# Optimization experiments

Hardware: AMD Instinct MI355X
Metric: run time of the kernel (lower is better)

Reference implementation:

```python
import jax, jax.numpy as jnp
import numpy as np
from functools import partial

T, B = 1000, 256
STATE_DIM, ACTION_DIM, REWARD_DIM = 64, 8, 1
EMBED = 64
HIDDEN = 256


def setup_inputs() -> dict:
    key = jax.random.key(0)
    ks = jax.random.split(key, 12)
    g = lambda k, shape, fan_in: jax.random.normal(k, shape, jnp.float32) * np.sqrt(2.0 / fan_in)
    return {
        "states": jax.random.normal(ks[0], (T, B, STATE_DIM), jnp.float32),
        "actions": jax.random.normal(ks[1], (T, B, ACTION_DIM), jnp.float32),
        "rewards": jax.random.normal(ks[2], (T, B, REWARD_DIM), jnp.float32),
        # embedding linears (VarianceScaling(2.0) init, zero bias)
        "Ws": g(ks[3], (STATE_DIM, EMBED), STATE_DIM), "bs": jnp.zeros((EMBED,), jnp.float32),
        "Wa": g(ks[4], (ACTION_DIM, EMBED), ACTION_DIM), "ba": jnp.zeros((EMBED,), jnp.float32),
        "Wr": g(ks[5], (REWARD_DIM, EMBED), REWARD_DIM), "br": jnp.zeros((EMBED,), jnp.float32),
        # hk.GRU params: w_i [in, 3H], w_h [H, 3H], b [3H]
        "wi": g(ks[6], (3 * EMBED, 3 * HIDDEN), 3 * EMBED),
        "wh": g(ks[7], (HIDDEN, 3 * HIDDEN), HIDDEN),
        "bg": jnp.zeros((3 * HIDDEN,), jnp.float32),
    }


def _gru_scan(x_seq, h0, wi, wh, bg):
    # x_seq: [T, B, 3*EMBED]; hk.GRU math: z,r = sigmoid gates; a = tanh candidate
    H = HIDDEN
    wh_zr, wh_a = wh[:, : 2 * H], wh[:, 2 * H :]
    b_zr, b_a = bg[: 2 * H], bg[2 * H :]

    def step(h, gx):  # gx = x @ wi precomputed, [B, 3H]
        zr = jax.nn.sigmoid(gx[:, : 2 * H] + h @ wh_zr + b_zr)
        z, r = zr[:, :H], zr[:, H:]
        a = jnp.tanh(gx[:, 2 * H :] + (r * h) @ wh_a + b_a)
        h_next = (1.0 - z) * h + z * a
        return h_next, h_next

    gx_seq = jnp.einsum("tbd,dh->tbh", x_seq, wi)  # one big matmul over all steps
    _, hs = jax.lax.scan(step, h0, gx_seq)
    return hs  # [T, B, H]


def reference(states, actions, rewards, Ws, bs, Wa, ba, Wr, br, wi, wh, bg):
    se = jax.nn.gelu(states @ Ws + bs)
    ae = jax.nn.gelu(actions @ Wa + ba)
    re = jax.nn.gelu(rewards @ Wr + br)
    x = jnp.concatenate((se, ae, re), axis=-1)  # [T, B, 3*EMBED]
    h0 = jnp.zeros((x.shape[1], HIDDEN), x.dtype)
    return _gru_scan(x, h0, wi, wh, bg)
```

## Files before the change

kernel.cpp:

```cpp
#include <hip/hip_runtime.h>
#include <hip/hip_bf16.h>

#define TT   1000
#define BB   256
#define HID  256
#define GD   768
#define XD   192
#define NROW (TT*BB)

typedef __attribute__((ext_vector_type(8))) _Float16 half8;
typedef __attribute__((ext_vector_type(4))) float    float4_t;
typedef __attribute__((ext_vector_type(2))) unsigned uint2_t;

#define MFMA16(A,B,C) __builtin_amdgcn_mfma_f32_16x16x32_f16((A),(B),(C),0,0,0)

__device__ __forceinline__ void gll16(const void* g, void* l) {
  __builtin_amdgcn_global_load_lds((const __attribute__((address_space(1))) void*)g,
                                   (__attribute__((address_space(3))) void*)l, 16, 0, 0);
}

__device__ __forceinline__ unsigned short f2h(float f) {
  _Float16 h = (_Float16)f;
  union { _Float16 h; unsigned short u; } c; c.h = h; return c.u;
}
__device__ __forceinline__ uint2_t pk4h(float4_t v) {
  union { _Float16 h[4]; uint2_t u; } c;
  c.h[0] = (_Float16)v.x; c.h[1] = (_Float16)v.y;
  c.h[2] = (_Float16)v.z; c.h[3] = (_Float16)v.w;
  return c.u;
}
__device__ __forceinline__ float4_t h4_to_f4(uint2_t v) {
  union { uint2_t u; _Float16 h[4]; } c; c.u = v;
  float4_t f;
  f.x = (float)c.h[0]; f.y = (float)c.h[1];
  f.z = (float)c.h[2]; f.w = (float)c.h[3];
  return f;
}
__device__ __forceinline__ float sigx(float x) {
  return __builtin_amdgcn_rcpf(1.0f + __builtin_amdgcn_exp2f(-1.4426950408889634f * x));
}
__device__ __forceinline__ float tanhx(float x) {
  return 1.0f - 2.0f * __builtin_amdgcn_rcpf(1.0f + __builtin_amdgcn_exp2f(2.8853900817779268f * x));
}
__device__ __forceinline__ float4_t sig4(float4_t v){ float4_t o; o.x=sigx(v.x); o.y=sigx(v.y); o.z=sigx(v.z); o.w=sigx(v.w); return o; }
__device__ __forceinline__ float4_t tanh4(float4_t v){ float4_t o; o.x=tanhx(v.x); o.y=tanhx(v.y); o.z=tanhx(v.z); o.w=tanhx(v.w); return o; }
__device__ __forceinline__ float gelu1(float v){
  float c = v + 0.044715f * v * v * v;
  float e = __builtin_amdgcn_exp2f((0.7978845608028654f * 2.8853900817779268f) * c);
  float th = 1.0f - 2.0f * __builtin_amdgcn_rcpf(1.0f + e);
  return 0.5f * v * (1.0f + th);
}

__global__ void k_prep(const float* __restrict__ wi, const float* __restrict__ wh,
                       unsigned short* __restrict__ wiT, unsigned short* __restrict__ whF)
{
  int tid = blockIdx.x * 256 + threadIdx.x;
  if (tid < GD*XD) {
    int n = tid / XD, k = tid - n*XD;
    wiT[tid] = f2h(wi[(size_t)k*GD + n]);
  }
  int t2 = tid - GD*XD;
  if (t2 >= 0 && t2 < 48*8*64*8) {
    int j = t2 & 7, l = (t2 >> 3) & 63, f = t2 >> 9;
    int mf = f >> 3, kf = f & 7;
    int k = kf*32 + ((l >> 4) << 3) + j;
    int n = (mf << 4) + (l & 15);
    whF[t2] = f2h(wh[(size_t)k*GD + n]);
  }
}

__global__ void k_embed(const float* __restrict__ st, const float* __restrict__ ac,
                        const float* __restrict__ rw,
                        const float* __restrict__ Ws, const float* __restrict__ bs,
                        const float* __restrict__ Wa, const float* __restrict__ ba,
                        const float* __restrict__ Wr, const float* __restrict__ br,
                        unsigned short* __restrict__ x)
{
  int lane = threadIdx.x & 63;
  int wid = blockIdx.x * (blockDim.x >> 6) + (threadIdx.x >> 6);
  int nw  = gridDim.x * (blockDim.x >> 6);
  float wsr[64], war[8];
  #pragma unroll
  for (int k = 0; k < 64; ++k) wsr[k] = Ws[k*64 + lane];
  #pragma unroll
  for (int k = 0; k < 8; ++k) war[k] = Wa[k*64 + lane];
  float wrr = Wr[lane];
  float bsv = bs[lane], bav = ba[lane], brv = br[lane];
  for (int row = wid; row < NROW; row += nw) {
    const float4_t* sp = (const float4_t*)(st + (size_t)row*64);
    float a0 = bsv;
    #pragma unroll
    for (int q = 0; q < 16; ++q) {
      float4_t v = sp[q];
      a0 = fmaf(v.x, wsr[4*q+0], a0);
      a0 = fmaf(v.y, wsr[4*q+1], a0);
      a0 = fmaf(v.z, wsr[4*q+2], a0);
      a0 = fmaf(v.w, wsr[4*q+3], a0);
    }
    const float4_t* ap = (const float4_t*)(ac + (size_t)row*8);
    float a1 = bav;
    #pragma unroll
    for (int q = 0; q < 2; ++q) {
      float4_t v = ap[q];
      a1 = fmaf(v.x, war[4*q+0], a1);
      a1 = fmaf(v.y, war[4*q+1], a1);
      a1 = fmaf(v.z, war[4*q+2], a1);
      a1 = fmaf(v.w, war[4*q+3], a1);
    }
    float a2 = fmaf(rw[row], wrr, brv);
    unsigned short* xr = x + (size_t)row*XD;
    xr[lane]       = f2h(gelu1(a0));
    xr[64 + lane]  = f2h(gelu1(a1));
    xr[128 + lane] = f2h(gelu1(a2));
  }
}

__global__ __launch_bounds__(512, 2) void k_gx(const unsigned short* __restrict__ x,
                                               const unsigned short* __restrict__ wiT,
                                               const float* __restrict__ bg,
                                               unsigned short* __restrict__ gx)
{
  __shared__ half8 Xs[24*64];
  __shared__ half8 As[16*64];
  int lane = threadIdx.x & 63;
  int wv   = threadIdx.x >> 6;
  int b    = lane & 15;
  int g8   = (lane >> 4) << 3;
  int row0 = blockIdx.x * 64;
  #pragma unroll
  for (int i = 0; i < 3; ++i) {
    int c = wv*3 + i, nf = c / 6, kf = c - nf*6;
    gll16(x + (size_t)(row0 + nf*16 + b)*XD + kf*32 + g8, &Xs[c*64]);
  }
  int g4 = g8 >> 1;
  float4_t acc[6][4];
  #pragma unroll
  for (int i = 0; i < 6; ++i) {
    float4_t bgv = *(const float4_t*)(bg + (wv + 8*i)*16 + g4);
    #pragma unroll
    for (int nf = 0; nf < 4; ++nf) acc[i][nf] = bgv;
  }
  half8 xb[4];
  for (int kf = 0; kf < 6; ++kf) {
    #pragma unroll
    for (int p = 0; p < 3; ++p) {
      __syncthreads();
      #pragma unroll
      for (int i2 = 0; i2 < 2; ++i2) {
        int q = wv*2 + i2;
        gll16(wiT + (size_t)((p*16 + q)*16 + b)*XD + kf*32 + g8, &As[q*64]);
      }
      __syncthreads();
      if (p == 0) {
        #pragma unroll
        for (int nf = 0; nf < 4; ++nf) xb[nf] = Xs[(nf*6 + kf)*64 + lane];
      }
      half8 af0 = As[wv*64 + lane];
      half8 af1 = As[(wv+8)*64 + lane];
      #pragma unroll
      for (int nf = 0; nf < 4; ++nf) {
        acc[2*p  ][nf] = MFMA16(af0, xb[nf], acc[2*p  ][nf]);
        acc[2*p+1][nf] = MFMA16(af1, xb[nf], acc[2*p+1][nf]);
      }
    }
  }
  char* gxc = (char*)gx;
  #pragma unroll
  for (int i = 0; i < 6; ++i) {
    #pragma unroll
    for (int nf = 0; nf < 4; ++nf) {
      size_t idx = (((size_t)blockIdx.x*48 + (wv + 8*i))*4 + nf)*512 + lane*8;
      *(uint2_t*)(gxc + idx) = pk4h(acc[i][nf]);
    }
  }
}

__global__
__attribute__((amdgpu_flat_work_group_size(512, 512), amdgpu_waves_per_eu(2, 2)))
void k_gru(const unsigned short* __restrict__ gx,
           const unsigned short* __restrict__ whF,
           float* __restrict__ out)
{
  __shared__ char smem[98304];
  char* h_lds  = smem;
  char* rh_lds = smem + 8448;
  char* gxb    = smem + 16896;
  const int tid  = threadIdx.x;
  const int lane = tid & 63;
  const int wv   = tid >> 6;
  const int wg   = blockIdx.x;
  const int b    = lane & 15;
  const int g    = lane >> 4;
  const int kr4  = g << 2;

  half8 wz0[8], wz1[8], wr0[8], wr1[8], wa0[8], wa1[8];
  #pragma unroll
  for (int kf = 0; kf < 8; ++kf) {
    wz0[kf] = *(const half8*)(whF + ((size_t)((( 2*wv    )*8 + kf)*64 + lane) << 3));
    wz1[kf] = *(const half8*)(whF + ((size_t)((( 2*wv + 1)*8 + kf)*64 + lane) << 3));
    wr0[kf] = *(const half8*)(whF + ((size_t)(((16 + 2*wv)*8 + kf)*64 + lane) << 3));
    wr1[kf] = *(const half8*)(whF + ((size_t)(((17 + 2*wv)*8 + kf)*64 + lane) << 3));
    wa0[kf] = *(const half8*)(whF + ((size_t)(((32 + 2*wv)*8 + kf)*64 + lane) << 3));
    wa1[kf] = *(const half8*)(whF + ((size_t)(((33 + 2*wv)*8 + kf)*64 + lane) << 3));
  }
  #pragma unroll
  for (int kf = 0; kf < 8; ++kf) {
    asm volatile("" : "+v"(wz0[kf]));
    asm volatile("" : "+v"(wz1[kf]));
    asm volatile("" : "+v"(wr0[kf]));
    asm volatile("" : "+v"(wr1[kf]));
    asm volatile("" : "+v"(wa0[kf]));
    asm volatile("" : "+v"(wa1[kf]));
  }
  for (int i = tid; i < 2112; i += 512) ((unsigned*)h_lds)[i] = 0u;

  const int nf   = wg & 3;
  const int bsel = wg >> 2;
  int soff[3], dch[3];
  #pragma unroll
  for (int i = 0; i < 3; ++i) {
    int c = i*16 + (tid >> 5);
    int r = (tid & 31) << 4;
    soff[i] = nf*512 + c*2048 + r;
    dch[i]  = i*8192 + tid*16;
  }
  const char* gxc = (const char*)gx;
  #pragma unroll
  for (int i = 0; i < 3; ++i)
    gll16(gxc + (size_t)bsel*98304 + soff[i], gxb + dch[i]);
  __syncthreads();

  float4_t hf0 = {0.f, 0.f, 0.f, 0.f}, hf1 = hf0;
  const char* hb_base = h_lds + b*528;
  const char* rb_base = rh_lds + b*528;
  const int off_h0 = (wv*32 + kr4) << 1;
  const int off_h1 = off_h0 + 32;
  const int lz0 = ( 2*wv    )*512 + lane*8;
  const int lz1 = ( 2*wv + 1)*512 + lane*8;
  const int lr0 = (16 + 2*wv)*512 + lane*8;
  const int lr1 = (17 + 2*wv)*512 + lane*8;
  const int la0 = (32 + 2*wv)*512 + lane*8;
  const int la1 = (33 + 2*wv)*512 + lane*8;

  for (int t = 0; t < TT; ++t) {
    asm volatile("s_waitcnt vmcnt(2) lgkmcnt(0)" ::: "memory");
    __builtin_amdgcn_s_barrier();
    asm volatile("" ::: "memory");
    if (t + 1 < TT) {
      const char* slab = gxc + ((size_t)(t+1)*4 + bsel)*98304;
      char* dstb = gxb + 24576*((t+1) & 1);
      #pragma unroll
      for (int i = 0; i < 3; ++i) gll16(slab + soff[i], dstb + dch[i]);
    }
    const char* cur = gxb + 24576*(t & 1);
    float4_t az0 = h4_to_f4(*(const uint2_t*)(cur + lz0));
    float4_t az1 = h4_to_f4(*(const uint2_t*)(cur + lz1));
    float4_t ar0 = h4_to_f4(*(const uint2_t*)(cur + lr0));
    float4_t ar1 = h4_to_f4(*(const uint2_t*)(cur + lr1));
    #pragma unroll
    for (int kf = 0; kf < 8; ++kf) {
      half8 hb = *(const half8*)(hb_base + kf*64 + (g << 4));
      az0 = MFMA16(wz0[kf], hb, az0);
      az1 = MFMA16(wz1[kf], hb, az1);
      ar0 = MFMA16(wr0[kf], hb, ar0);
      ar1 = MFMA16(wr1[kf], hb, ar1);
    }
    float4_t z0 = sig4(az0), z1 = sig4(az1);
    float4_t rh0 = sig4(ar0) * hf0, rh1 = sig4(ar1) * hf1;
    *(uint2_t*)(rh_lds + b*528 + off_h0) = pk4h(rh0);
    *(uint2_t*)(rh_lds + b*528 + off_h1) = pk4h(rh1);
    asm volatile("s_waitcnt lgkmcnt(0)" ::: "memory");
    __builtin_amdgcn_s_barrier();
    asm volatile("" ::: "memory");
    float4_t aa0 = h4_to_f4(*(const uint2_t*)(cur + la0));
    float4_t aa1 = h4_to_f4(*(const uint2_t*)(cur + la1));
    #pragma unroll
    for (int kf = 0; kf < 8; ++kf) {
      half8 rb = *(const half8*)(rb_base + kf*64 + (g << 4));
      aa0 = MFMA16(wa0[kf], rb, aa0);
      aa1 = MFMA16(wa1[kf], rb, aa1);
    }
    float4_t a0 = tanh4(aa0), a1 = tanh4(aa1);
    float4_t hn0 = hf0 + z0 * (a0 - hf0);
    float4_t hn1 = hf1 + z1 * (a1 - hf1);
    hf0 = hn0; hf1 = hn1;
    *(uint2_t*)(h_lds + b*528 + off_h0) = pk4h(hn0);
    *(uint2_t*)(h_lds + b*528 + off_h1) = pk4h(hn1);
    float* op = out + (((size_t)t*BB + wg*16 + b) << 8) + wv*32 + kr4;
    *(float4_t*)op = hn0;
    *(float4_t*)(op + 16) = hn1;
  }
}

extern "C" void kernel_launch(void* const* d_in, const int* in_sizes, int n_in,
                              void* d_out, int out_size, void* d_ws, size_t ws_size,
                              hipStream_t stream) {
  (void)in_sizes; (void)n_in; (void)out_size; (void)ws_size;
  const float* states  = (const float*)d_in[0];
  const float* actions = (const float*)d_in[1];
  const float* rewards = (const float*)d_in[2];
  const float* Ws = (const float*)d_in[3];
  const float* bs = (const float*)d_in[4];
  const float* Wa = (const float*)d_in[5];
  const float* ba = (const float*)d_in[6];
  const float* Wr = (const float*)d_in[7];
  const float* br = (const float*)d_in[8];
  const float* wi = (const float*)d_in[9];
  const float* wh = (const float*)d_in[10];
  const float* bg = (const float*)d_in[11];
  char* wsb = (char*)d_ws;
  unsigned short* gx  = (unsigned short*)(wsb);
  unsigned short* x   = (unsigned short*)(wsb + 393216000LL);
  unsigned short* wiT = (unsigned short*)(wsb + 491520000LL);
  unsigned short* whF = (unsigned short*)(wsb + 491814912LL);
  k_prep <<<1344, 256, 0, stream>>>(wi, wh, wiT, whF);
  k_embed<<<1000, 256, 0, stream>>>(states, actions, rewards, Ws, bs, Wa, ba, Wr, br, x);
  k_gx   <<<4000, 512, 0, stream>>>(x, wiT, bg, gx);
  k_gru  <<<16, 512, 0, stream>>>(gx, whF, (float*)d_out);
}
```

Measured before the change: 2.186 ms.

## Pin z/r recurrent weights in AGPRs and stream candidate weights from global

Moves the z and r gate weight fragments out of VGPRs into fixed AGPRs (a0-a127) with inline asm and feeds them straight to hand-written MFMA sequences. The candidate-gate weights are no longer kept resident; they are reloaded from global memory (expected to hit in cache) every timestep, with the loads issued early to overlap the gate math and barrier. The aim is to relieve VGPR pressure and control MFMA scheduling. In exchange it adds per-step global traffic and manual s_nop hazard padding, and the loaded operand layout must match the previous fragment layout exactly.

Result: slower. 2.874 ms (+31.5%).

```diff
diff --git a/kernel.cpp b/kernel.cpp
--- a/kernel.cpp
+++ b/kernel.cpp
@@ -13,6 +13,18 @@
 typedef __attribute__((ext_vector_type(2))) unsigned uint2_t;
 
 #define MFMA16(A,B,C) __builtin_amdgcn_mfma_f32_16x16x32_f16((A),(B),(C),0,0,0)
+
+#define ACLOB \
+  "a0","a1","a2","a3","a4","a5","a6","a7","a8","a9","a10","a11","a12","a13","a14","a15", \
+  "a16","a17","a18","a19","a20","a21","a22","a23","a24","a25","a26","a27","a28","a29","a30","a31", \
+  "a32","a33","a34","a35","a36","a37","a38","a39","a40","a41","a42","a43","a44","a45","a46","a47", \
+  "a48","a49","a50","a51","a52","a53","a54","a55","a56","a57","a58","a59","a60","a61","a62","a63", \
+  "a64","a65","a66","a67","a68","a69","a70","a71","a72","a73","a74","a75","a76","a77","a78","a79", \
+  "a80","a81","a82","a83","a84","a85","a86","a87","a88","a89","a90","a91","a92","a93","a94","a95", \
+  "a96","a97","a98","a99","a100","a101","a102","a103","a104","a105","a106","a107","a108","a109","a110","a111", \
+  "a112","a113","a114","a115","a116","a117","a118","a119","a120","a121","a122","a123","a124","a125","a126","a127"
+
+union h8u4 { half8 h; unsigned u[4]; };
 
 __device__ __forceinline__ void gll16(const void* g, void* l) {
   __builtin_amdgcn_global_load_lds((const __attribute__((address_space(1))) void*)g,
@@ -192,26 +204,33 @@
   const int b    = lane & 15;
   const int g    = lane >> 4;
   const int kr4  = g << 2;
-
-  half8 wz0[8], wz1[8], wr0[8], wr1[8], wa0[8], wa1[8];
-  #pragma unroll
-  for (int kf = 0; kf < 8; ++kf) {
-    wz0[kf] = *(const half8*)(whF + ((size_t)((( 2*wv    )*8 + kf)*64 + lane) << 3));
-    wz1[kf] = *(const half8*)(whF + ((size_t)((( 2*wv + 1)*8 + kf)*64 + lane) << 3));
-    wr0[kf] = *(const half8*)(whF + ((size_t)(((16 + 2*wv)*8 + kf)*64 + lane) << 3));
-    wr1[kf] = *(const half8*)(whF + ((size_t)(((17 + 2*wv)*8 + kf)*64 + lane) << 3));
-    wa0[kf] = *(const half8*)(whF + ((size_t)(((32 + 2*wv)*8 + kf)*64 + lane) << 3));
-    wa1[kf] = *(const half8*)(whF + ((size_t)(((33 + 2*wv)*8 + kf)*64 + lane) << 3));
-  }
-  #pragma unroll
-  for (int kf = 0; kf < 8; ++kf) {
-    asm volatile("" : "+v"(wz0[kf]));
-    asm volatile("" : "+v"(wz1[kf]));
-    asm volatile("" : "+v"(wr0[kf]));
-    asm volatile("" : "+v"(wr1[kf]));
-    asm volatile("" : "+v"(wa0[kf]));
-    asm volatile("" : "+v"(wa1[kf]));
-  }
+  const int g16  = g << 4;
+
+#define PIN(FK, S0,S1,S2,S3) do { h8u4 _c; \
+    _c.h = *(const half8*)(whF + ((size_t)((FK)*64 + lane) << 3)); \
+    asm volatile("v_accvgpr_write_b32 a" S0 ", %0\n\t" \
+                 "v_accvgpr_write_b32 a" S1 ", %1\n\t" \
+                 "v_accvgpr_write_b32 a" S2 ", %2\n\t" \
+                 "v_accvgpr_write_b32 a" S3 ", %3" \
+                 :: "v"(_c.u[0]), "v"(_c.u[1]), "v"(_c.u[2]), "v"(_c.u[3]) : ACLOB); } while(0)
+  PIN(16*wv+0,  "0","1","2","3");     PIN(16*wv+1,  "4","5","6","7");
+  PIN(16*wv+2,  "8","9","10","11");   PIN(16*wv+3,  "12","13","14","15");
+  PIN(16*wv+4,  "16","17","18","19"); PIN(16*wv+5,  "20","21","22","23");
+  PIN(16*wv+6,  "24","25","26","27"); PIN(16*wv+7,  "28","29","30","31");
+  PIN(16*wv+8,  "32","33","34","35"); PIN(16*wv+9,  "36","37","38","39");
+  PIN(16*wv+10, "40","41","42","43"); PIN(16*wv+11, "44","45","46","47");
+  PIN(16*wv+12, "48","49","50","51"); PIN(16*wv+13, "52","53","54","55");
+  PIN(16*wv+14, "56","57","58","59"); PIN(16*wv+15, "60","61","62","63");
+  PIN(128+16*wv+0, "64","65","66","67");   PIN(128+16*wv+1, "68","69","70","71");
+  PIN(128+16*wv+2, "72","73","74","75");   PIN(128+16*wv+3, "76","77","78","79");
+  PIN(128+16*wv+4, "80","81","82","83");   PIN(128+16*wv+5, "84","85","86","87");
+  PIN(128+16*wv+6, "88","89","90","91");   PIN(128+16*wv+7, "92","93","94","95");
+  PIN(136+16*wv+0, "96","97","98","99");    PIN(136+16*wv+1, "100","101","102","103");
+  PIN(136+16*wv+2, "104","105","106","107");PIN(136+16*wv+3, "108","109","110","111");
+  PIN(136+16*wv+4, "112","113","114","115");PIN(136+16*wv+5, "116","117","118","119");
+  PIN(136+16*wv+6, "120","121","122","123");PIN(136+16*wv+7, "124","125","126","127");
+#undef PIN
+
   for (int i = tid; i < 2112; i += 512) ((unsigned*)h_lds)[i] = 0u;
 
   const int nf   = wg & 3;
@@ -241,9 +260,10 @@
   const int lr1 = (17 + 2*wv)*512 + lane*8;
   const int la0 = (32 + 2*wv)*512 + lane*8;
   const int la1 = (33 + 2*wv)*512 + lane*8;
+  const unsigned short* wap = whF;
 
   for (int t = 0; t < TT; ++t) {
-    asm volatile("s_waitcnt vmcnt(2) lgkmcnt(0)" ::: "memory");
+    asm volatile("s_waitcnt vmcnt(2) lgkmcnt(0)" ::: "memory", ACLOB);
     __builtin_amdgcn_s_barrier();
     asm volatile("" ::: "memory");
     if (t + 1 < TT) {
@@ -257,29 +277,121 @@
     float4_t az1 = h4_to_f4(*(const uint2_t*)(cur + lz1));
     float4_t ar0 = h4_to_f4(*(const uint2_t*)(cur + lr0));
     float4_t ar1 = h4_to_f4(*(const uint2_t*)(cur + lr1));
-    #pragma unroll
-    for (int kf = 0; kf < 8; ++kf) {
-      half8 hb = *(const half8*)(hb_base + kf*64 + (g << 4));
-      az0 = MFMA16(wz0[kf], hb, az0);
-      az1 = MFMA16(wz1[kf], hb, az1);
-      ar0 = MFMA16(wr0[kf], hb, ar0);
-      ar1 = MFMA16(wr1[kf], hb, ar1);
-    }
+    half8 hb0 = *(const half8*)(hb_base + 0*64 + g16);
+    half8 hb1 = *(const half8*)(hb_base + 1*64 + g16);
+    half8 hb2 = *(const half8*)(hb_base + 2*64 + g16);
+    half8 hb3 = *(const half8*)(hb_base + 3*64 + g16);
+    half8 hb4 = *(const half8*)(hb_base + 4*64 + g16);
+    half8 hb5 = *(const half8*)(hb_base + 5*64 + g16);
+    half8 hb6 = *(const half8*)(hb_base + 6*64 + g16);
+    half8 hb7 = *(const half8*)(hb_base + 7*64 + g16);
+    asm volatile(
+      "s_nop 1\n\t"
+      "v_mfma_f32_16x16x32_f16 %0, a[0:3], %4, %0\n\t"
+      "v_mfma_f32_16x16x32_f16 %1, a[32:35], %4, %1\n\t"
+      "v_mfma_f32_16x16x32_f16 %2, a[64:67], %4, %2\n\t"
+      "v_mfma_f32_16x16x32_f16 %3, a[96:99], %4, %3\n\t"
+      "v_mfma_f32_16x16x32_f16 %0, a[4:7], %5, %0\n\t"
+      "v_mfma_f32_16x16x32_f16 %1, a[36:39], %5, %1\n\t"
+      "v_mfma_f32_16x16x32_f16 %2, a[68:71], %5, %2\n\t"
+      "v_mfma_f32_16x16x32_f16 %3, a[100:103], %5, %3\n\t"
+      "v_mfma_f32_16x16x32_f16 %0, a[8:11], %6, %0\n\t"
+      "v_mfma_f32_16x16x32_f16 %1, a[40:43], %6, %1\n\t"
+      "v_mfma_f32_16x16x32_f16 %2, a[72:75], %6, %2\n\t"
+      "v_mfma_f32_16x16x32_f16 %3, a[104:107], %6, %3\n\t"
+      "v_mfma_f32_16x16x32_f16 %0, a[12:15], %7, %0\n\t"
+      "v_mfma_f32_16x16x32_f16 %1, a[44:47], %7, %1\n\t"
+      "v_mfma_f32_16x16x32_f16 %2, a[76:79], %7, %2\n\t"
+      "v_mfma_f32_16x16x32_f16 %3, a[108:111], %7, %3\n\t"
+      "v_mfma_f32_16x16x32_f16 %0, a[16:19], %8, %0\n\t"
+      "v_mfma_f32_16x16x32_f16 %1, a[48:51], %8, %1\n\t"
+      "v_mfma_f32_16x16x32_f16 %2, a[80:83], %8, %2\n\t"
+      "v_mfma_f32_16x16x32_f16 %3, a[112:115], %8, %3\n\t"
+      "v_mfma_f32_16x16x32_f16 %0, a[20:23], %9, %0\n\t"
+      "v_mfma_f32_16x16x32_f16 %1, a[52:55], %9, %1\n\t"
+      "v_mfma_f32_16x16x32_f16 %2, a[84:87], %9, %2\n\t"
+      "v_mfma_f32_16x16x32_f16 %3, a[116:119], %9, %3\n\t"
+      "v_mfma_f32_16x16x32_f16 %0, a[24:27], %10, %0\n\t"
+      "v_mfma_f32_16x16x32_f16 %1, a[56:59], %10, %1\n\t"
+      "v_mfma_f32_16x16x32_f16 %2, a[88:91], %10, %2\n\t"
+      "v_mfma_f32_16x16x32_f16 %3, a[120:123], %10, %3\n\t"
+      "v_mfma_f32_16x16x32_f16 %0, a[28:31], %11, %0\n\t"
+      "v_mfma_f32_16x16x32_f16 %1, a[60:63], %11, %1\n\t"
+      "v_mfma_f32_16x16x32_f16 %2, a[92:95], %11, %2\n\t"
+      "v_mfma_f32_16x16x32_f16 %3, a[124:127], %11, %3\n\t"
+      "s_nop 7\n\t"
+      "s_nop 7"
+      : "+v"(az0), "+v"(az1), "+v"(ar0), "+v"(ar1)
+      : "v"(hb0), "v"(hb1), "v"(hb2), "v"(hb3),
+        "v"(hb4), "v"(hb5), "v"(hb6), "v"(hb7)
+      : ACLOB);
+    __builtin_amdgcn_sched_barrier(0);
+    asm volatile("" : "+s"(wap));
+    half8 wa00 = *(const half8*)(wap + ((size_t)((256+16*wv+0)*64 + lane) << 3));
+    half8 wa01 = *(const half8*)(wap + ((size_t)((256+16*wv+1)*64 + lane) << 3));
+    half8 wa02 = *(const half8*)(wap + ((size_t)((256+16*wv+2)*64 + lane) << 3));
+    half8 wa03 = *(const half8*)(wap + ((size_t)((256+16*wv+3)*64 + lane) << 3));
+    half8 wa04 = *(const half8*)(wap + ((size_t)((256+16*wv+4)*64 + lane) << 3));
+    half8 wa05 = *(const half8*)(wap + ((size_t)((256+16*wv+5)*64 + lane) << 3));
+    half8 wa06 = *(const half8*)(wap + ((size_t)((256+16*wv+6)*64 + lane) << 3));
+    half8 wa07 = *(const half8*)(wap + ((size_t)((256+16*wv+7)*64 + lane) << 3));
+    half8 wa10 = *(const half8*)(wap + ((size_t)((264+16*wv+0)*64 + lane) << 3));
+    half8 wa11 = *(const half8*)(wap + ((size_t)((264+16*wv+1)*64 + lane) << 3));
+    half8 wa12 = *(const half8*)(wap + ((size_t)((264+16*wv+2)*64 + lane) << 3));
+    half8 wa13 = *(const half8*)(wap + ((size_t)((264+16*wv+3)*64 + lane) << 3));
+    half8 wa14 = *(const half8*)(wap + ((size_t)((264+16*wv+4)*64 + lane) << 3));
+    half8 wa15 = *(const half8*)(wap + ((size_t)((264+16*wv+5)*64 + lane) << 3));
+    half8 wa16 = *(const half8*)(wap + ((size_t)((264+16*wv+6)*64 + lane) << 3));
+    half8 wa17 = *(const half8*)(wap + ((size_t)((264+16*wv+7)*64 + lane) << 3));
     float4_t z0 = sig4(az0), z1 = sig4(az1);
     float4_t rh0 = sig4(ar0) * hf0, rh1 = sig4(ar1) * hf1;
     *(uint2_t*)(rh_lds + b*528 + off_h0) = pk4h(rh0);
     *(uint2_t*)(rh_lds + b*528 + off_h1) = pk4h(rh1);
-    asm volatile("s_waitcnt lgkmcnt(0)" ::: "memory");
+    asm volatile("s_waitcnt lgkmcnt(0)" ::: "memory", ACLOB);
     __builtin_amdgcn_s_barrier();
     asm volatile("" ::: "memory");
     float4_t aa0 = h4_to_f4(*(const uint2_t*)(cur + la0));
     float4_t aa1 = h4_to_f4(*(const uint2_t*)(cur + la1));
-    #pragma unroll
-    for (int kf = 0; kf < 8; ++kf) {
-      half8 rb = *(const half8*)(rb_base + kf*64 + (g << 4));
-      aa0 = MFMA16(wa0[kf], rb, aa0);
-      aa1 = MFMA16(wa1[kf], rb, aa1);
-    }
+    half8 rb0 = *(const half8*)(rb_base + 0*64 + g16);
+    half8 rb1 = *(const half8*)(rb_base + 1*64 + g16);
+    half8 rb2 = *(const half8*)(rb_base + 2*64 + g16);
+    half8 rb3 = *(const half8*)(rb_base + 3*64 + g16);
+    asm volatile(
+      "s_nop 2\n\t"
+      "v_mfma_f32_16x16x32_f16 %0, %2, %10, %0\n\t"
+      "v_mfma_f32_16x16x32_f16 %1, %6, %10, %1\n\t"
+      "v_mfma_f32_16x16x32_f16 %0, %3, %11, %0\n\t"
+      "v_mfma_f32_16x16x32_f16 %1, %7, %11, %1\n\t"
+      "v_mfma_f32_16x16x32_f16 %0, %4, %12, %0\n\t"
+      "v_mfma_f32_16x16x32_f16 %1, %8, %12, %1\n\t"
+      "v_mfma_f32_16x16x32_f16 %0, %5, %13, %0\n\t"
+      "v_mfma_f32_16x16x32_f16 %1, %9, %13, %1"
+      : "+v"(aa0), "+v"(aa1)
+      : "v"(wa00), "v"(wa01), "v"(wa02), "v"(wa03),
+        "v"(wa10), "v"(wa11), "v"(wa12), "v"(wa13),
+        "v"(rb0), "v"(rb1), "v"(rb2), "v"(rb3)
+      : ACLOB);
+    half8 rb4 = *(const half8*)(rb_base + 4*64 + g16);
+    half8 rb5 = *(const half8*)(rb_base + 5*64 + g16);
+    half8 rb6 = *(const half8*)(rb_base + 6*64 + g16);
+    half8 rb7 = *(const half8*)(rb_base + 7*64 + g16);
+    asm volatile(
+      "s_nop 2\n\t"
+      "v_mfma_f32_16x16x32_f16 %0, %2, %10, %0\n\t"
+      "v_mfma_f32_16x16x32_f16 %1, %6, %10, %1\n\t"
+      "v_mfma_f32_16x16x32_f16 %0, %3, %11, %0\n\t"
+      "v_mfma_f32_16x16x32_f16 %1, %7, %11, %1\n\t"
+      "v_mfma_f32_16x16x32_f16 %0, %4, %12, %0\n\t"
+      "v_mfma_f32_16x16x32_f16 %1, %8, %12, %1\n\t"
+      "v_mfma_f32_16x16x32_f16 %0, %5, %13, %0\n\t"
+      "v_mfma_f32_16x16x32_f16 %1, %9, %13, %1\n\t"
+      "s_nop 7\n\t"
+      "s_nop 7"
+      : "+v"(aa0), "+v"(aa1)
+      : "v"(wa04), "v"(wa05), "v"(wa06), "v"(wa07),
+        "v"(wa14), "v"(wa15), "v"(wa16), "v"(wa17),
+        "v"(rb4), "v"(rb5), "v"(rb6), "v"(rb7)
+      : ACLOB);
     float4_t a0 = tanh4(aa0), a1 = tanh4(aa1);
     float4_t hn0 = hf0 + z0 * (a0 - hf0);
     float4_t hn1 = hf1 + z1 * (a1 - hf1);
```

## Pin recurrent weights in AGPRs and stream z-gate weights from global each step

Applied to the files above, without the earlier changes.

Moves the r-gate and candidate recurrent weight fragments into explicitly written AGPRs and issues the MFMAs through inline assembly that reads those registers directly. The z-gate weights are no longer kept resident and are reloaded from global memory (L2) every timestep into VGPRs. The gx prefetch now runs unconditionally so the vmcnt accounting stays consistent. The intent is to relieve VGPR pressure and spilling at two waves per EU. In exchange it adds global load latency on the serial critical path every step, and it relies on hand-placed s_nop padding for MFMA hazards and on clobber lists to keep the compiler out of the AGPRs.

New measurement: 3.401 ms. 1.56x slower.

```diff
diff --git a/kernel.cpp b/kernel.cpp
--- a/kernel.cpp
+++ b/kernel.cpp
@@ -13,6 +13,18 @@
 typedef __attribute__((ext_vector_type(2))) unsigned uint2_t;
 
 #define MFMA16(A,B,C) __builtin_amdgcn_mfma_f32_16x16x32_f16((A),(B),(C),0,0,0)
+
+#define ACLOB \
+  "a0","a1","a2","a3","a4","a5","a6","a7","a8","a9","a10","a11","a12","a13","a14","a15", \
+  "a16","a17","a18","a19","a20","a21","a22","a23","a24","a25","a26","a27","a28","a29","a30","a31", \
+  "a32","a33","a34","a35","a36","a37","a38","a39","a40","a41","a42","a43","a44","a45","a46","a47", \
+  "a48","a49","a50","a51","a52","a53","a54","a55","a56","a57","a58","a59","a60","a61","a62","a63", \
+  "a64","a65","a66","a67","a68","a69","a70","a71","a72","a73","a74","a75","a76","a77","a78","a79", \
+  "a80","a81","a82","a83","a84","a85","a86","a87","a88","a89","a90","a91","a92","a93","a94","a95", \
+  "a96","a97","a98","a99","a100","a101","a102","a103","a104","a105","a106","a107","a108","a109","a110","a111", \
+  "a112","a113","a114","a115","a116","a117","a118","a119","a120","a121","a122","a123","a124","a125","a126","a127"
+
+union h8u4 { half8 h; unsigned u[4]; };
 
 __device__ __forceinline__ void gll16(const void* g, void* l) {
   __builtin_amdgcn_global_load_lds((const __attribute__((address_space(1))) void*)g,
@@ -192,27 +204,40 @@
   const int b    = lane & 15;
   const int g    = lane >> 4;
   const int kr4  = g << 2;
-
-  half8 wz0[8], wz1[8], wr0[8], wr1[8], wa0[8], wa1[8];
-  #pragma unroll
-  for (int kf = 0; kf < 8; ++kf) {
-    wz0[kf] = *(const half8*)(whF + ((size_t)((( 2*wv    )*8 + kf)*64 + lane) << 3));
-    wz1[kf] = *(const half8*)(whF + ((size_t)((( 2*wv + 1)*8 + kf)*64 + lane) << 3));
-    wr0[kf] = *(const half8*)(whF + ((size_t)(((16 + 2*wv)*8 + kf)*64 + lane) << 3));
-    wr1[kf] = *(const half8*)(whF + ((size_t)(((17 + 2*wv)*8 + kf)*64 + lane) << 3));
-    wa0[kf] = *(const half8*)(whF + ((size_t)(((32 + 2*wv)*8 + kf)*64 + lane) << 3));
-    wa1[kf] = *(const half8*)(whF + ((size_t)(((33 + 2*wv)*8 + kf)*64 + lane) << 3));
-  }
-  #pragma unroll
-  for (int kf = 0; kf < 8; ++kf) {
-    asm volatile("" : "+v"(wz0[kf]));
-    asm volatile("" : "+v"(wz1[kf]));
-    asm volatile("" : "+v"(wr0[kf]));
-    asm volatile("" : "+v"(wr1[kf]));
-    asm volatile("" : "+v"(wa0[kf]));
-    asm volatile("" : "+v"(wa1[kf]));
-  }
+  const int g16  = g << 4;
+
+#define PIN(FK, S0,S1,S2,S3) do { h8u4 _c; \
+    _c.h = *(const half8*)(whF + ((size_t)((FK)*64 + lane) << 3)); \
+    asm volatile("v_accvgpr_write_b32 a" S0 ", %0\n\t" \
+                 "v_accvgpr_write_b32 a" S1 ", %1\n\t" \
+                 "v_accvgpr_write_b32 a" S2 ", %2\n\t" \
+                 "v_accvgpr_write_b32 a" S3 ", %3" \
+                 :: "v"(_c.u[0]), "v"(_c.u[1]), "v"(_c.u[2]), "v"(_c.u[3]) : ACLOB); } while(0)
+  PIN(128+16*wv+0, "0","1","2","3");     PIN(128+16*wv+1, "4","5","6","7");
+  PIN(128+16*wv+2, "8","9","10","11");   PIN(128+16*wv+3, "12","13","14","15");
+  PIN(128+16*wv+4, "16","17","18","19"); PIN(128+16*wv+5, "20","21","22","23");
+  PIN(128+16*wv+6, "24","25","26","27"); PIN(128+16*wv+7, "28","29","30","31");
+  PIN(136+16*wv+0, "32","33","34","35"); PIN(136+16*wv+1, "36","37","38","39");
+  PIN(136+16*wv+2, "40","41","42","43"); PIN(136+16*wv+3, "44","45","46","47");
+  PIN(136+16*wv+4, "48","49","50","51"); PIN(136+16*wv+5, "52","53","54","55");
+  PIN(136+16*wv+6, "56","57","58","59"); PIN(136+16*wv+7, "60","61","62","63");
+  PIN(256+16*wv+0, "64","65","66","67");   PIN(256+16*wv+1, "68","69","70","71");
+  PIN(256+16*wv+2, "72","73","74","75");   PIN(256+16*wv+3, "76","77","78","79");
+  PIN(256+16*wv+4, "80","81","82","83");   PIN(256+16*wv+5, "84","85","86","87");
+  PIN(256+16*wv+6, "88","89","90","91");   PIN(256+16*wv+7, "92","93","94","95");
+  PIN(264+16*wv+0, "96","97","98","99");    PIN(264+16*wv+1, "100","101","102","103");
+  PIN(264+16*wv+2, "104","105","106","107");PIN(264+16*wv+3, "108","109","110","111");
+  PIN(264+16*wv+4, "112","113","114","115");PIN(264+16*wv+5, "116","117","118","119");
+  PIN(264+16*wv+6, "120","121","122","123");PIN(264+16*wv+7, "124","125","126","127");
+#undef PIN
+
   for (int i = tid; i < 2112; i += 512) ((unsigned*)h_lds)[i] = 0u;
+
+  const unsigned long long wzb0 =
+      (unsigned long long)(const char*)(whF + ((size_t)((16*wv)*64 + lane) << 3));
+  const unsigned long long wzb1 = wzb0 + 4096;
+  const unsigned long long wzb2 = wzb0 + 8192;
+  const unsigned long long wzb3 = wzb0 + 12288;
 
   const int nf   = wg & 3;
   const int bsel = wg >> 2;
@@ -243,43 +268,146 @@
   const int la1 = (33 + 2*wv)*512 + lane*8;
 
   for (int t = 0; t < TT; ++t) {
-    asm volatile("s_waitcnt vmcnt(2) lgkmcnt(0)" ::: "memory");
+    asm volatile("s_waitcnt vmcnt(2) lgkmcnt(0)" ::: "memory", ACLOB);
     __builtin_amdgcn_s_barrier();
     asm volatile("" ::: "memory");
-    if (t + 1 < TT) {
-      const char* slab = gxc + ((size_t)(t+1)*4 + bsel)*98304;
+
+    half8 za0, za1, za2, za3, za4, za5, za6, za7;
+    half8 zb0, zb1, zb2, zb3, zb4, zb5, zb6, zb7;
+    asm volatile("global_load_dwordx4 %0, %1, off"             : "=v"(za0) : "v"(wzb0));
+    asm volatile("global_load_dwordx4 %0, %1, off offset:1024" : "=v"(za1) : "v"(wzb0));
+    asm volatile("global_load_dwordx4 %0, %1, off offset:2048" : "=v"(za2) : "v"(wzb0));
+    asm volatile("global_load_dwordx4 %0, %1, off offset:3072" : "=v"(za3) : "v"(wzb0));
+    asm volatile("global_load_dwordx4 %0, %1, off"             : "=v"(za4) : "v"(wzb1));
+    asm volatile("global_load_dwordx4 %0, %1, off offset:1024" : "=v"(za5) : "v"(wzb1));
+    asm volatile("global_load_dwordx4 %0, %1, off offset:2048" : "=v"(za6) : "v"(wzb1));
+    asm volatile("global_load_dwordx4 %0, %1, off offset:3072" : "=v"(za7) : "v"(wzb1));
+    asm volatile("global_load_dwordx4 %0, %1, off"             : "=v"(zb0) : "v"(wzb2));
+    asm volatile("global_load_dwordx4 %0, %1, off offset:1024" : "=v"(zb1) : "v"(wzb2));
+    asm volatile("global_load_dwordx4 %0, %1, off offset:2048" : "=v"(zb2) : "v"(wzb2));
+    asm volatile("global_load_dwordx4 %0, %1, off offset:3072" : "=v"(zb3) : "v"(wzb2));
+    asm volatile("global_load_dwordx4 %0, %1, off"             : "=v"(zb4) : "v"(wzb3));
+    asm volatile("global_load_dwordx4 %0, %1, off offset:1024" : "=v"(zb5) : "v"(wzb3));
+    asm volatile("global_load_dwordx4 %0, %1, off offset:2048" : "=v"(zb6) : "v"(wzb3));
+    asm volatile("global_load_dwordx4 %0, %1, off offset:3072" : "=v"(zb7) : "v"(wzb3));
+
+    {
+      int tn = (t + 1 < TT) ? (t + 1) : t;
+      const char* slab = gxc + ((size_t)tn*4 + bsel)*98304;
       char* dstb = gxb + 24576*((t+1) & 1);
       #pragma unroll
       for (int i = 0; i < 3; ++i) gll16(slab + soff[i], dstb + dch[i]);
     }
+
     const char* cur = gxb + 24576*(t & 1);
     float4_t az0 = h4_to_f4(*(const uint2_t*)(cur + lz0));
     float4_t az1 = h4_to_f4(*(const uint2_t*)(cur + lz1));
     float4_t ar0 = h4_to_f4(*(const uint2_t*)(cur + lr0));
     float4_t ar1 = h4_to_f4(*(const uint2_t*)(cur + lr1));
-    #pragma unroll
-    for (int kf = 0; kf < 8; ++kf) {
-      half8 hb = *(const half8*)(hb_base + kf*64 + (g << 4));
-      az0 = MFMA16(wz0[kf], hb, az0);
-      az1 = MFMA16(wz1[kf], hb, az1);
-      ar0 = MFMA16(wr0[kf], hb, ar0);
-      ar1 = MFMA16(wr1[kf], hb, ar1);
-    }
+    half8 hb0 = *(const half8*)(hb_base + 0*64 + g16);
+    half8 hb1 = *(const half8*)(hb_base + 1*64 + g16);
+    asm volatile(
+      "s_waitcnt vmcnt(3)\n\t"
+      "s_nop 2\n\t"
+      "v_mfma_f32_16x16x32_f16 %0, %4, %8, %0\n\t"
+      "v_mfma_f32_16x16x32_f16 %1, %5, %8, %1\n\t"
+      "v_mfma_f32_16x16x32_f16 %2, a[0:3], %8, %2\n\t"
+      "v_mfma_f32_16x16x32_f16 %3, a[32:35], %8, %3\n\t"
+      "v_mfma_f32_16x16x32_f16 %0, %6, %9, %0\n\t"
+      "v_mfma_f32_16x16x32_f16 %1, %7, %9, %1\n\t"
+      "v_mfma_f32_16x16x32_f16 %2, a[4:7], %9, %2\n\t"
+      "v_mfma_f32_16x16x32_f16 %3, a[36:39], %9, %3"
+      : "+v"(az0), "+v"(az1), "+v"(ar0), "+v"(ar1)
+      : "v"(za0), "v"(zb0), "v"(za1), "v"(zb1), "v"(hb0), "v"(hb1)
+      : ACLOB);
+    half8 hb2 = *(const half8*)(hb_base + 2*64 + g16);
+    half8 hb3 = *(const half8*)(hb_base + 3*64 + g16);
+    asm volatile(
+      "v_mfma_f32_16x16x32_f16 %0, %4, %8, %0\n\t"
+      "v_mfma_f32_16x16x32_f16 %1, %5, %8, %1\n\t"
+      "v_mfma_f32_16x16x32_f16 %2, a[8:11], %8, %2\n\t"
+      "v_mfma_f32_16x16x32_f16 %3, a[40:43], %8, %3\n\t"
+      "v_mfma_f32_16x16x32_f16 %0, %6, %9, %0\n\t"
+      "v_mfma_f32_16x16x32_f16 %1, %7, %9, %1\n\t"
+      "v_mfma_f32_16x16x32_f16 %2, a[12:15], %9, %2\n\t"
+      "v_mfma_f32_16x16x32_f16 %3, a[44:47], %9, %3"
+      : "+v"(az0), "+v"(az1), "+v"(ar0), "+v"(ar1)
+      : "v"(za2), "v"(zb2), "v"(za3), "v"(zb3), "v"(hb2), "v"(hb3)
+      : ACLOB);
+    half8 hb4 = *(const half8*)(hb_base + 4*64 + g16);
+    half8 hb5 = *(const half8*)(hb_base + 5*64 + g16);
+    asm volatile(
+      "v_mfma_f32_16x16x32_f16 %0, %4, %8, %0\n\t"
+      "v_mfma_f32_16x16x32_f16 %1, %5, %8, %1\n\t"
+      "v_mfma_f32_16x16x32_f16 %2, a[16:19], %8, %2\n\t"
+      "v_mfma_f32_16x16x32_f16 %3, a[48:51], %8, %3\n\t"
+      "v_mfma_f32_16x16x32_f16 %0, %6, %9, %0\n\t"
+      "v_mfma_f32_16x16x32_f16 %1, %7, %9, %1\n\t"
+      "v_mfma_f32_16x16x32_f16 %2, a[20:23], %9, %2\n\t"
+      "v_mfma_f32_16x16x32_f16 %3, a[52:55], %9, %3"
+      : "+v"(az0), "+v"(az1), "+v"(ar0), "+v"(ar1)
+      : "v"(za4), "v"(zb4), "v"(za5), "v"(zb5), "v"(hb4), "v"(hb5)
+      : ACLOB);
+    half8 hb6 = *(const half8*)(hb_base + 6*64 + g16);
+    half8 hb7 = *(const half8*)(hb_base + 7*64 + g16);
+    asm volatile(
+      "v_mfma_f32_16x16x32_f16 %0, %4, %8, %0\n\t"
+      "v_mfma_f32_16x16x32_f16 %1, %5, %8, %1\n\t"
+      "v_mfma_f32_16x16x32_f16 %2, a[24:27], %8, %2\n\t"
+      "v_mfma_f32_16x16x32_f16 %3, a[56:59], %8, %3\n\t"
+      "v_mfma_f32_16x16x32_f16 %0, %6, %9, %0\n\t"
+      "v_mfma_f32_16x16x32_f16 %1, %7, %9, %1\n\t"
+      "v_mfma_f32_16x16x32_f16 %2, a[28:31], %9, %2\n\t"
+      "v_mfma_f32_16x16x32_f16 %3, a[60:63], %9, %3\n\t"
+      "s_nop 7\n\t"
+      "s_nop 7"
+      : "+v"(az0), "+v"(az1), "+v"(ar0), "+v"(ar1)
+      : "v"(za6), "v"(zb6), "v"(za7), "v"(zb7), "v"(hb6), "v"(hb7)
+      : ACLOB);
     float4_t z0 = sig4(az0), z1 = sig4(az1);
     float4_t rh0 = sig4(ar0) * hf0, rh1 = sig4(ar1) * hf1;
     *(uint2_t*)(rh_lds + b*528 + off_h0) = pk4h(rh0);
     *(uint2_t*)(rh_lds + b*528 + off_h1) = pk4h(rh1);
-    asm volatile("s_waitcnt lgkmcnt(0)" ::: "memory");
+    asm volatile("s_waitcnt lgkmcnt(0)" ::: "memory", ACLOB);
     __builtin_amdgcn_s_barrier();
     asm volatile("" ::: "memory");
     float4_t aa0 = h4_to_f4(*(const uint2_t*)(cur + la0));
     float4_t aa1 = h4_to_f4(*(const uint2_t*)(cur + la1));
-    #pragma unroll
-    for (int kf = 0; kf < 8; ++kf) {
-      half8 rb = *(const half8*)(rb_base + kf*64 + (g << 4));
-      aa0 = MFMA16(wa0[kf], rb, aa0);
-      aa1 = MFMA16(wa1[kf], rb, aa1);
-    }
+    half8 rb0 = *(const half8*)(rb_base + 0*64 + g16);
+    half8 rb1 = *(const half8*)(rb_base + 1*64 + g16);
+    half8 rb2 = *(const half8*)(rb_base + 2*64 + g16);
+    half8 rb3 = *(const half8*)(rb_base + 3*64 + g16);
+    asm volatile(
+      "s_nop 2\n\t"
+      "v_mfma_f32_16x16x32_f16 %0, a[64:67], %2, %0\n\t"
+      "v_mfma_f32_16x16x32_f16 %1, a[96:99], %2, %1\n\t"
+      "v_mfma_f32_16x16x32_f16 %0, a[68:71], %3, %0\n\t"
+      "v_mfma_f32_16x16x32_f16 %1, a[100:103], %3, %1\n\t"
+      "v_mfma_f32_16x16x32_f16 %0, a[72:75], %4, %0\n\t"
+      "v_mfma_f32_16x16x32_f16 %1, a[104:107], %4, %1\n\t"
+      "v_mfma_f32_16x16x32_f16 %0, a[76:79], %5, %0\n\t"
+      "v_mfma_f32_16x16x32_f16 %1, a[108:111], %5, %1"
+      : "+v"(aa0), "+v"(aa1)
+      : "v"(rb0), "v"(rb1), "v"(rb2), "v"(rb3)
+      : ACLOB);
+    half8 rb4 = *(const half8*)(rb_base + 4*64 + g16);
+    half8 rb5 = *(const half8*)(rb_base + 5*64 + g16);
+    half8 rb6 = *(const half8*)(rb_base + 6*64 + g16);
+    half8 rb7 = *(const half8*)(rb_base + 7*64 + g16);
+    asm volatile(
+      "v_mfma_f32_16x16x32_f16 %0, a[80:83], %2, %0\n\t"
+      "v_mfma_f32_16x16x32_f16 %1, a[112:115], %2, %1\n\t"
+      "v_mfma_f32_16x16x32_f16 %0, a[84:87], %3, %0\n\t"
+      "v_mfma_f32_16x16x32_f16 %1, a[116:119], %3, %1\n\t"
+      "v_mfma_f32_16x16x32_f16 %0, a[88:91], %4, %0\n\t"
+      "v_mfma_f32_16x16x32_f16 %1, a[120:123], %4, %1\n\t"
+      "v_mfma_f32_16x16x32_f16 %0, a[92:95], %5, %0\n\t"
+      "v_mfma_f32_16x16x32_f16 %1, a[124:127], %5, %1\n\t"
+      "s_nop 7\n\t"
+      "s_nop 7"
+      : "+v"(aa0), "+v"(aa1)
+      : "v"(rb4), "v"(rb5), "v"(rb6), "v"(rb7)
+      : ACLOB);
     float4_t a0 = tanh4(aa0), a1 = tanh4(aa1);
     float4_t hn0 = hf0 + z0 * (a0 - hf0);
     float4_t hn1 = hf1 + z1 * (a1 - hf1);
```
